# Performance work log

Hardware: AMD Instinct MI355X
Metric: run time of the kernel (lower is better)

Reference implementation:

```python
import jax, jax.numpy as jnp
import numpy as np
import math

B, S, D = 2, 512, 768
N_HEADS, HEAD = 12, 64
ALPHA = 32.0


def setup_inputs() -> dict:
    key = jax.random.key(0)
    ks = jax.random.split(key, 12)
    w_scale = 1.0 / math.sqrt(D)
    return {
        "hidden_states": jax.random.normal(ks[0], (B, S, D), jnp.float32),
        "attention_mask": jnp.zeros((B, 1, 1, S), jnp.float32),
        "rel_pos": jax.random.normal(ks[1], (B, S, S, HEAD), jnp.float32),
        "rel_2d_pos": jax.random.normal(ks[2], (B, S, S, HEAD), jnp.float32),
        "rel_2d_angle": jax.random.normal(ks[3], (B, S, S, HEAD), jnp.float32),
        "Wq": jax.random.normal(ks[4], (D, D), jnp.float32) * w_scale,
        "bq": jnp.zeros((D,), jnp.float32),
        "Wk": jax.random.normal(ks[5], (D, D), jnp.float32) * w_scale,
        "bk": jnp.zeros((D,), jnp.float32),
        "Wv": jax.random.normal(ks[6], (D, D), jnp.float32) * w_scale,
        "bv": jnp.zeros((D,), jnp.float32),
    }


def _heads(x):
    # (B,S,D) -> (B,N,S,HEAD)
    b, s, _ = x.shape
    return x.reshape(b, s, N_HEADS, HEAD).transpose(0, 2, 1, 3)


def reference(hidden_states, attention_mask, rel_pos, rel_2d_pos, rel_2d_angle,
              Wq, bq, Wk, bk, Wv, bv):
    q = _heads(hidden_states @ Wq.T + bq)
    k = _heads(hidden_states @ Wk.T + bk)
    v = _heads(hidden_states @ Wv.T + bv)

    qs = q / math.sqrt(HEAD)  # scaled query, (B,N,S,HEAD)
    scores = jnp.einsum('bnsh,bnkh->bnsk', qs, k)
    scores = scores + jnp.einsum('bnsh,bskh->bnsk', qs, rel_pos)
    scores = scores + jnp.einsum('bnsh,bskh->bnsk', qs, rel_2d_pos)
    scores = scores + jnp.einsum('bnsh,bskh->bnsk', qs, rel_2d_angle)
    scores = scores + attention_mask

    # cogview (PB-Relax) softmax: subtract per-row max of scores/alpha, rescale
    scaled = scores / ALPHA
    m = jnp.max(scaled, axis=-1, keepdims=True)
    probs = jax.nn.softmax((scaled - m) * ALPHA, axis=-1)

    ctx = jnp.einsum('bnsk,bnkh->bsnh', probs, v)  # (B,S,N,HEAD)
    return ctx.reshape(ctx.shape[0], ctx.shape[1], N_HEADS * HEAD)
```

## Files before the change

### kernel.cpp

```cpp
#include <hip/hip_runtime.h>

typedef __attribute__((ext_vector_type(8))) short short8;
typedef __attribute__((ext_vector_type(4))) float f32x4;

#define B_ 2
#define S_ 512
#define D_ 768
#define NH 12
#define HD 64

__device__ inline short f2bf(float f) {
    union { float f; unsigned u; } v; v.f = f;
    unsigned r = v.u + 0x7fffu + ((v.u >> 16) & 1u);
    return (short)(r >> 16);
}

__device__ __forceinline__ f32x4 ntload4(const float* p) {
    return __builtin_nontemporal_load((const f32x4*)p);
}

__global__ __launch_bounds__(256) void qkv_gemm(
    const float* __restrict__ hidden,
    const float* __restrict__ Wq, const float* __restrict__ Wk, const float* __restrict__ Wv,
    const float* __restrict__ bq, const float* __restrict__ bk, const float* __restrict__ bv,
    short* __restrict__ qbf, short* __restrict__ kbf, short* __restrict__ vbf)
{
    __shared__ short hs[64 * 72];
    __shared__ short wt[64 * 72];

    const int mt = blockIdx.x, nt = blockIdx.y, mat = blockIdx.z;
    const int m0 = mt * 64, n0 = nt * 64;
    const float* W    = (mat == 0) ? Wq : ((mat == 1) ? Wk : Wv);
    const float* bias = (mat == 0) ? bq : ((mat == 1) ? bk : bv);

    const int tid = threadIdx.x;
    const int w = tid >> 6, l = tid & 63;
    const int sr = tid >> 2, sc = (tid & 3) * 16;

    f32x4 acc[4];
    #pragma unroll
    for (int i = 0; i < 4; ++i) acc[i] = (f32x4){0.f, 0.f, 0.f, 0.f};

    const int arow = (w * 16 + (l & 15)) * 72 + (l >> 4) * 8;

    for (int kt = 0; kt < 12; ++kt) {
        const int d0 = kt * 64;
        if (kt) __syncthreads();
        {
            const float4* sa = (const float4*)(hidden + (size_t)(m0 + sr) * D_ + d0 + sc);
            float4 x0 = sa[0], x1 = sa[1], x2 = sa[2], x3 = sa[3];
            short8 p0 = {f2bf(x0.x), f2bf(x0.y), f2bf(x0.z), f2bf(x0.w),
                         f2bf(x1.x), f2bf(x1.y), f2bf(x1.z), f2bf(x1.w)};
            short8 p1 = {f2bf(x2.x), f2bf(x2.y), f2bf(x2.z), f2bf(x2.w),
                         f2bf(x3.x), f2bf(x3.y), f2bf(x3.z), f2bf(x3.w)};
            *(short8*)&hs[sr * 72 + sc]     = p0;
            *(short8*)&hs[sr * 72 + sc + 8] = p1;
            const float4* sb = (const float4*)(W + (size_t)(n0 + sr) * D_ + d0 + sc);
            float4 y0 = sb[0], y1 = sb[1], y2 = sb[2], y3 = sb[3];
            short8 q0 = {f2bf(y0.x), f2bf(y0.y), f2bf(y0.z), f2bf(y0.w),
                         f2bf(y1.x), f2bf(y1.y), f2bf(y1.z), f2bf(y1.w)};
            short8 q1 = {f2bf(y2.x), f2bf(y2.y), f2bf(y2.z), f2bf(y2.w),
                         f2bf(y3.x), f2bf(y3.y), f2bf(y3.z), f2bf(y3.w)};
            *(short8*)&wt[sr * 72 + sc]     = q0;
            *(short8*)&wt[sr * 72 + sc + 8] = q1;
        }
        __syncthreads();
        short8 a0 = *(const short8*)&hs[arow];
        short8 a1 = *(const short8*)&hs[arow + 32];
        #pragma unroll
        for (int ct = 0; ct < 4; ++ct) {
            const int brow = (ct * 16 + (l & 15)) * 72 + (l >> 4) * 8;
            short8 b0 = *(const short8*)&wt[brow];
            short8 b1 = *(const short8*)&wt[brow + 32];
            acc[ct] = __builtin_amdgcn_mfma_f32_16x16x32_bf16(a0, b0, acc[ct], 0, 0, 0);
            acc[ct] = __builtin_amdgcn_mfma_f32_16x16x32_bf16(a1, b1, acc[ct], 0, 0, 0);
        }
    }

    if (mat == 2) {
        __syncthreads();
        #pragma unroll
        for (int ct = 0; ct < 4; ++ct) {
            #pragma unroll
            for (int rr = 0; rr < 4; ++rr) {
                const int m_l = w * 16 + (l >> 4) * 4 + rr;
                const int n_l = ct * 16 + (l & 15);
                hs[n_l * 68 + m_l] = f2bf(acc[ct][rr] + bias[n0 + n_l]);
            }
        }
        __syncthreads();
        const int b   = m0 >> 9;
        const int s0b = m0 & 511;
        #pragma unroll
        for (int j = 0; j < 2; ++j) {
            const int idx  = j * 256 + tid;
            const int h    = idx >> 3;
            const int sseg = (idx & 7) * 8;
            short8 vv = *(const short8*)&hs[h * 68 + sseg];
            *(short8*)(vbf + ((size_t)(b * NH + nt) * HD + h) * S_ + s0b + sseg) = vv;
        }
    } else {
        #pragma unroll
        for (int ct = 0; ct < 4; ++ct) {
            #pragma unroll
            for (int rr = 0; rr < 4; ++rr) {
                const int m_l = w * 16 + (l >> 4) * 4 + rr;
                const int n_l = ct * 16 + (l & 15);
                const int m = m0 + m_l;
                const int b = m >> 9, s = m & 511;
                float v = acc[ct][rr] + bias[n0 + n_l];
                const size_t dst = (((size_t)(b * NH + nt) * S_) + s) * HD + n_l;
                if (mat == 0) qbf[dst] = f2bf(v * 0.125f);
                else          kbf[dst] = f2bf(v);
            }
        }
    }
}

__global__ __launch_bounds__(256) void score_rel(
    const short* __restrict__ qbf,
    const float* __restrict__ rel1, const float* __restrict__ rel2, const float* __restrict__ rel3,
    float* __restrict__ relsc)
{
    const int kt = blockIdx.x;
    const int s  = blockIdx.y;
    const int b  = blockIdx.z;
    const int tid = threadIdx.x;
    const int w = tid >> 6, l = tid & 63;

    const int rowsel = l & 15;
    const int hc     = (l >> 4) * 8;

    const int kc = kt * 4 + w;
    const size_t rbase = ((size_t)(b * S_ + s)) * S_ * HD;
    const size_t ro = rbase + (size_t)(kc * 16 + rowsel) * HD + hc;

    f32x4 p0a = ntload4(rel1 + ro);
    f32x4 p0b = ntload4(rel1 + ro + 4);
    f32x4 q0a = ntload4(rel1 + ro + 32);
    f32x4 q0b = ntload4(rel1 + ro + 36);
    f32x4 p1a = ntload4(rel2 + ro);
    f32x4 p1b = ntload4(rel2 + ro + 4);
    f32x4 q1a = ntload4(rel2 + ro + 32);
    f32x4 q1b = ntload4(rel2 + ro + 36);
    f32x4 p2a = ntload4(rel3 + ro);
    f32x4 p2b = ntload4(rel3 + ro + 4);
    f32x4 q2a = ntload4(rel3 + ro + 32);
    f32x4 q2b = ntload4(rel3 + ro + 36);

    short8 a0 = {0, 0, 0, 0, 0, 0, 0, 0};
    short8 a1 = {0, 0, 0, 0, 0, 0, 0, 0};
    if (rowsel < NH) {
        const short* qp = qbf + (((size_t)(b * NH + rowsel) * S_) + s) * HD;
        a0 = *(const short8*)(qp + hc);
        a1 = *(const short8*)(qp + hc + 32);
    }

    short8 b0 = {
        f2bf(p0a.x + p1a.x + p2a.x), f2bf(p0a.y + p1a.y + p2a.y),
        f2bf(p0a.z + p1a.z + p2a.z), f2bf(p0a.w + p1a.w + p2a.w),
        f2bf(p0b.x + p1b.x + p2b.x), f2bf(p0b.y + p1b.y + p2b.y),
        f2bf(p0b.z + p1b.z + p2b.z), f2bf(p0b.w + p1b.w + p2b.w)};
    short8 b1 = {
        f2bf(q0a.x + q1a.x + q2a.x), f2bf(q0a.y + q1a.y + q2a.y),
        f2bf(q0a.z + q1a.z + q2a.z), f2bf(q0a.w + q1a.w + q2a.w),
        f2bf(q0b.x + q1b.x + q2b.x), f2bf(q0b.y + q1b.y + q2b.y),
        f2bf(q0b.z + q1b.z + q2b.z), f2bf(q0b.w + q1b.w + q2b.w)};

    f32x4 acc = (f32x4){0.f, 0.f, 0.f, 0.f};
    acc = __builtin_amdgcn_mfma_f32_16x16x32_bf16(a0, b0, acc, 0, 0, 0);
    acc = __builtin_amdgcn_mfma_f32_16x16x32_bf16(a1, b1, acc, 0, 0, 0);

    const int kg = kc * 16 + rowsel;
    #pragma unroll
    for (int rr = 0; rr < 4; ++rr) {
        const int n = (l >> 4) * 4 + rr;
        if (n < NH)
            relsc[(((size_t)(b * S_ + s)) * NH + n) * S_ + kg] = acc[rr];
    }
}

__global__ __launch_bounds__(256) void smqkpv(
    const short* __restrict__ qbf, const short* __restrict__ kbf,
    const float* __restrict__ relsc, const float* __restrict__ mask,
    const short* __restrict__ vbf, float* __restrict__ out)
{
    __shared__ float sc[16][520];
    __shared__ short pbf[16][520];

    const int st  = blockIdx.x;
    const int n   = blockIdx.y;
    const int b   = blockIdx.z;
    const int s0  = st * 16;
    const int tid = threadIdx.x;
    const int w = tid >> 6, l = tid & 63;

    const int arow = l & 15;
    const int g    = l >> 4;

    const short* qp = qbf + (((size_t)(b * NH + n) * S_) + s0 + arow) * HD + g * 8;
    short8 a0 = *(const short8*)(qp);
    short8 a1 = *(const short8*)(qp + 32);

    f32x4 acc[8];
    #pragma unroll
    for (int t = 0; t < 8; ++t) acc[t] = (f32x4){0.f, 0.f, 0.f, 0.f};

    #pragma unroll
    for (int t = 0; t < 8; ++t) {
        const int k0 = (w * 8 + t) * 16;
        const short* kp = kbf + (((size_t)(b * NH + n) * S_) + k0 + arow) * HD + g * 8;
        short8 b0 = *(const short8*)(kp);
        short8 b1 = *(const short8*)(kp + 32);
        acc[t] = __builtin_amdgcn_mfma_f32_16x16x32_bf16(a0, b0, acc[t], 0, 0, 0);
        acc[t] = __builtin_amdgcn_mfma_f32_16x16x32_bf16(a1, b1, acc[t], 0, 0, 0);
    }

    #pragma unroll
    for (int t = 0; t < 8; ++t) {
        const int k0 = (w * 8 + t) * 16;
        #pragma unroll
        for (int rr = 0; rr < 4; ++rr)
            sc[g * 4 + rr][k0 + arow] = acc[t][rr];
    }
    __syncthreads();

    #pragma unroll
    for (int j = 0; j < 8; ++j) {
        const int fidx = j * 256 + tid;
        const int row  = fidx >> 7;
        const int c4   = (fidx & 127) * 4;
        float4 r = *(const float4*)(relsc +
                    (((size_t)(b * S_ + s0 + row)) * NH + n) * S_ + c4);
        float4 mk = *(const float4*)(mask + b * S_ + c4);
        float4 cur = *(const float4*)&sc[row][c4];
        cur.x += r.x + mk.x; cur.y += r.y + mk.y;
        cur.z += r.z + mk.z; cur.w += r.w + mk.w;
        *(float4*)&sc[row][c4] = cur;
    }
    __syncthreads();

    const int lane = l;
    for (int r = 0; r < 4; ++r) {
        const int row = w * 4 + r;
        float vals[8];
        float m = -1e30f;
        #pragma unroll
        for (int i = 0; i < 8; ++i) { vals[i] = sc[row][lane + 64 * i]; m = fmaxf(m, vals[i]); }
        #pragma unroll
        for (int off = 32; off >= 1; off >>= 1) m = fmaxf(m, __shfl_xor(m, off));
        float sum = 0.f;
        #pragma unroll
        for (int i = 0; i < 8; ++i) { vals[i] = __expf(vals[i] - m); sum += vals[i]; }
        #pragma unroll
        for (int off = 32; off >= 1; off >>= 1) sum += __shfl_xor(sum, off);
        const float inv = 1.0f / sum;
        #pragma unroll
        for (int i = 0; i < 8; ++i) pbf[row][lane + 64 * i] = f2bf(vals[i] * inv);
    }
    __syncthreads();

    f32x4 pacc = (f32x4){0.f, 0.f, 0.f, 0.f};
    const short* vrow = vbf + ((size_t)(b * NH + n) * HD + w * 16 + arow) * S_ + g * 8;
    #pragma unroll
    for (int kk = 0; kk < 16; ++kk) {
        short8 aP = *(const short8*)&pbf[arow][kk * 32 + g * 8];
        short8 bV = *(const short8*)(vrow + kk * 32);
        pacc = __builtin_amdgcn_mfma_f32_16x16x32_bf16(aP, bV, pacc, 0, 0, 0);
    }
    #pragma unroll
    for (int rr = 0; rr < 4; ++rr) {
        const int srow = g * 4 + rr;
        out[((size_t)(b * S_ + s0 + srow)) * D_ + n * HD + w * 16 + arow] = pacc[rr];
    }
}

extern "C" void kernel_launch(void* const* d_in, const int* in_sizes, int n_in,
                              void* d_out, int out_size, void* d_ws, size_t ws_size,
                              hipStream_t stream) {
    const float* hidden = (const float*)d_in[0];
    const float* mask   = (const float*)d_in[1];
    const float* rel1   = (const float*)d_in[2];
    const float* rel2   = (const float*)d_in[3];
    const float* rel3   = (const float*)d_in[4];
    const float* Wq     = (const float*)d_in[5];
    const float* bq     = (const float*)d_in[6];
    const float* Wk     = (const float*)d_in[7];
    const float* bk     = (const float*)d_in[8];
    const float* Wv     = (const float*)d_in[9];
    const float* bv     = (const float*)d_in[10];
    float* out = (float*)d_out;

    const size_t per = (size_t)B_ * NH * S_ * HD;
    short* qbf   = (short*)d_ws;
    short* kbf   = qbf + per;
    short* vbf   = kbf + per;
    float* relsc = (float*)(vbf + per);

    qkv_gemm<<<dim3(16, 12, 3), 256, 0, stream>>>(hidden, Wq, Wk, Wv, bq, bk, bv, qbf, kbf, vbf);
    score_rel<<<dim3(8, S_, B_), 256, 0, stream>>>(qbf, rel1, rel2, rel3, relsc);
    smqkpv<<<dim3(S_ / 16, NH, B_), 256, 0, stream>>>(qbf, kbf, relsc, mask, vbf, out);
}
```

Measured before the change: 128.9 us.

## Store relative-position scores and QK scores as bf16, fuse bias add into softmax

The intermediate relative-position score buffer is stored as bf16 instead of fp32, which halves its write traffic in score_rel and its read traffic in the attention kernel. The QK score tile in shared memory also becomes bf16, and the separate pass that added rel scores and mask into shared memory is folded into the softmax read loop, removing one shared-memory round trip and one barrier. The f2bf helper switches to the HIP intrinsic conversion. This rounds the scores to bf16 before softmax, which adds precision error that softmax with alpha=32 scaling may amplify.

```diff
diff --git a/kernel.cpp b/kernel.cpp
--- a/kernel.cpp
+++ b/kernel.cpp
@@ -1,4 +1,5 @@
 #include <hip/hip_runtime.h>
+#include <hip/hip_bf16.h>
 
 typedef __attribute__((ext_vector_type(8))) short short8;
 typedef __attribute__((ext_vector_type(4))) float f32x4;
@@ -9,10 +10,16 @@
 #define NH 12
 #define HD 64
 
-__device__ inline short f2bf(float f) {
-    union { float f; unsigned u; } v; v.f = f;
-    unsigned r = v.u + 0x7fffu + ((v.u >> 16) & 1u);
-    return (short)(r >> 16);
+__device__ __forceinline__ short f2bf(float f) {
+    union { __hip_bfloat16 h; short s; } u;
+    u.h = __float2bfloat16(f);
+    return u.s;
+}
+
+__device__ __forceinline__ float bf2f(short s) {
+    union { unsigned u; float f; } v;
+    v.u = ((unsigned)(unsigned short)s) << 16;
+    return v.f;
 }
 
 __device__ __forceinline__ f32x4 ntload4(const float* p) {
@@ -100,6 +107,7 @@
             *(short8*)(vbf + ((size_t)(b * NH + nt) * HD + h) * S_ + s0b + sseg) = vv;
         }
     } else {
+        const float sca = (mat == 0) ? 0.125f : 1.0f;
         #pragma unroll
         for (int ct = 0; ct < 4; ++ct) {
             #pragma unroll
@@ -108,9 +116,9 @@
                 const int n_l = ct * 16 + (l & 15);
                 const int m = m0 + m_l;
                 const int b = m >> 9, s = m & 511;
-                float v = acc[ct][rr] + bias[n0 + n_l];
+                float v = (acc[ct][rr] + bias[n0 + n_l]) * sca;
                 const size_t dst = (((size_t)(b * NH + nt) * S_) + s) * HD + n_l;
-                if (mat == 0) qbf[dst] = f2bf(v * 0.125f);
+                if (mat == 0) qbf[dst] = f2bf(v);
                 else          kbf[dst] = f2bf(v);
             }
         }
@@ -120,7 +128,7 @@
 __global__ __launch_bounds__(256) void score_rel(
     const short* __restrict__ qbf,
     const float* __restrict__ rel1, const float* __restrict__ rel2, const float* __restrict__ rel3,
-    float* __restrict__ relsc)
+    short* __restrict__ relsc)
 {
     const int kt = blockIdx.x;
     const int s  = blockIdx.y;
@@ -176,17 +184,17 @@
     for (int rr = 0; rr < 4; ++rr) {
         const int n = (l >> 4) * 4 + rr;
         if (n < NH)
-            relsc[(((size_t)(b * S_ + s)) * NH + n) * S_ + kg] = acc[rr];
+            relsc[(((size_t)(b * S_ + s)) * NH + n) * S_ + kg] = f2bf(acc[rr]);
     }
 }
 
 __global__ __launch_bounds__(256) void smqkpv(
     const short* __restrict__ qbf, const short* __restrict__ kbf,
-    const float* __restrict__ relsc, const float* __restrict__ mask,
+    const short* __restrict__ relsc, const float* __restrict__ mask,
     const short* __restrict__ vbf, float* __restrict__ out)
 {
-    __shared__ float sc[16][520];
-    __shared__ short pbf[16][520];
+    __shared__ short scb[16][520];
+    __shared__ short pbf[16][524];
 
     const int st  = blockIdx.x;
     const int n   = blockIdx.y;
@@ -221,32 +229,20 @@
         const int k0 = (w * 8 + t) * 16;
         #pragma unroll
         for (int rr = 0; rr < 4; ++rr)
-            sc[g * 4 + rr][k0 + arow] = acc[t][rr];
+            scb[g * 4 + rr][k0 + arow] = f2bf(acc[t][rr]);
     }
     __syncthreads();
 
-    #pragma unroll
-    for (int j = 0; j < 8; ++j) {
-        const int fidx = j * 256 + tid;
-        const int row  = fidx >> 7;
-        const int c4   = (fidx & 127) * 4;
-        float4 r = *(const float4*)(relsc +
-                    (((size_t)(b * S_ + s0 + row)) * NH + n) * S_ + c4);
-        float4 mk = *(const float4*)(mask + b * S_ + c4);
-        float4 cur = *(const float4*)&sc[row][c4];
-        cur.x += r.x + mk.x; cur.y += r.y + mk.y;
-        cur.z += r.z + mk.z; cur.w += r.w + mk.w;
-        *(float4*)&sc[row][c4] = cur;
-    }
-    __syncthreads();
-
-    const int lane = l;
     for (int r = 0; r < 4; ++r) {
         const int row = w * 4 + r;
+        const short* rp = relsc + (((size_t)(b * S_ + s0 + row)) * NH + n) * S_;
         float vals[8];
         float m = -1e30f;
         #pragma unroll
-        for (int i = 0; i < 8; ++i) { vals[i] = sc[row][lane + 64 * i]; m = fmaxf(m, vals[i]); }
+        for (int i = 0; i < 8; ++i) {
+            vals[i] = bf2f(scb[row][l + 64 * i]) + bf2f(rp[l + 64 * i]) + mask[b * S_ + l + 64 * i];
+            m = fmaxf(m, vals[i]);
+        }
         #pragma unroll
         for (int off = 32; off >= 1; off >>= 1) m = fmaxf(m, __shfl_xor(m, off));
         float sum = 0.f;
@@ -256,7 +252,7 @@
         for (int off = 32; off >= 1; off >>= 1) sum += __shfl_xor(sum, off);
         const float inv = 1.0f / sum;
         #pragma unroll
-        for (int i = 0; i < 8; ++i) pbf[row][lane + 64 * i] = f2bf(vals[i] * inv);
+        for (int i = 0; i < 8; ++i) pbf[row][l + 64 * i] = f2bf(vals[i] * inv);
     }
     __syncthreads();
 
@@ -295,7 +291,7 @@
     short* qbf   = (short*)d_ws;
     short* kbf   = qbf + per;
     short* vbf   = kbf + per;
-    float* relsc = (float*)(vbf + per);
+    short* relsc = vbf + per;
 
     qkv_gemm<<<dim3(16, 12, 3), 256, 0, stream>>>(hidden, Wq, Wk, Wv, bq, bk, bv, qbf, kbf, vbf);
     score_rel<<<dim3(8, S_, B_), 256, 0, stream>>>(qbf, rel1, rel2, rel3, relsc);
```

Result: no change. 126.9 us (median of 2 runs) (-1.5%).
